# Kernel optimization log

Hardware: AMD Instinct MI355X
Metric: run time of the kernel (lower is better)

The kernel has to match this reference:

```python
import jax, jax.numpy as jnp
import numpy as np

B, H, N, D, R, HIDDEN = 4, 12, 1025, 64, 1, 32


def _make_tables(N, R):
    # Geometry tables, mirroring FlexAttentionCPB.init_tables
    P = N - R
    S = int(P ** 0.5)
    assert S * S == P
    rng = np.arange(-(S - 1), S, dtype=np.float32)        # [2S-1]
    dY, dX = np.meshgrid(rng, rng, indexing='ij')
    rel = np.stack([dY / max(S - 1, 1), dX / max(S - 1, 1)], axis=-1).reshape(-1, 2)
    rel_table = np.sign(rel) * np.log1p(np.abs(rel))      # [(2S-1)^2, 2]
    yy = np.arange(S)
    Y, X = np.meshgrid(yy, yy, indexing='ij')
    flat = np.stack([Y, X], 0).reshape(2, -1)             # [2, P]
    d = (flat[:, :, None] - flat[:, None, :]).transpose(1, 2, 0).copy()  # [P,P,2]
    d[:, :, 0] += S - 1
    d[:, :, 1] += S - 1
    d[:, :, 0] *= 2 * S - 1
    l_idx = d.sum(-1).astype(np.int32)
    idx = np.full((N, N), -1, dtype=np.int32)
    idx[R:, R:] = l_idx
    return jnp.asarray(rel_table, jnp.float32), jnp.asarray(idx)


def setup_inputs() -> dict:
    key = jax.random.key(0)
    ks = jax.random.split(key, 8)
    rel_table, idx_table = _make_tables(N, R)
    return {
        'q': jax.random.normal(ks[0], (B, H, N, D), jnp.float32),
        'k': jax.random.normal(ks[1], (B, H, N, D), jnp.float32),
        'v': jax.random.normal(ks[2], (B, H, N, D), jnp.float32),
        'mu': jax.random.normal(ks[3], (B, H, 2, N), jnp.float32),
        'w1': jax.random.normal(ks[4], (2, HIDDEN), jnp.float32) * 0.5,
        'b1': jax.random.normal(ks[5], (HIDDEN,), jnp.float32) * 0.05,
        'w2': jax.random.normal(ks[6], (HIDDEN, H), jnp.float32) * 0.1,
        'gamma': jnp.zeros((H,), jnp.float32),   # nn.Parameter(torch.zeros(H))
        'rel_table': rel_table,
        'idx_table': idx_table,
    }


def reference(q, k, v, mu, w1, b1, w2, gamma, rel_table, idx_table):
    d = q.shape[-1]
    # CPB MLP: Linear(2,hidden)+GELU(exact)+Linear(hidden,H,no bias) -> [L,H]
    bt = jax.nn.gelu(rel_table @ w1 + b1, approximate=False) @ w2
    has_bias = (idx_table >= 0)                       # [N,N] == (q>=R)&(kv>=R)
    idx_c = jnp.where(has_bias, idx_table, 0)
    bias = jnp.transpose(bt[idx_c], (2, 0, 1))        # [H,N,N]
    mu_q = mu[:, :, 0, :]                             # [B,H,N]
    mu_k = mu[:, :, 1, :]
    gate = jax.nn.sigmoid(gamma)[None, :, None, None] * (
        mu_q[..., :, None] + mu_k[..., None, :])      # [B,H,N,N]
    scale = 1.0 / jnp.sqrt(jnp.asarray(d, q.dtype))
    scores = jnp.einsum('bhqd,bhkd->bhqk', q, k) * scale
    scores = scores + has_bias[None, None].astype(scores.dtype) * gate * bias[None]
    attn = jax.nn.softmax(scores, axis=-1)
    return jnp.einsum('bhqk,bhkd->bhqd', attn, v)
```

## Files before the change

### kernel.cpp

```cpp
#include <hip/hip_runtime.h>
#include <math.h>

#define B_ 4
#define H_ 12
#define N_ 1025
#define D_ 64
#define HID_ 32
#define TBL_ 3969
#define NQT 17
#define NBLK (B_ * H_ * NQT)
#define LOG2E 1.44269504f
#define THR_ 12.0f

typedef _Float16 half8 __attribute__((ext_vector_type(8)));
typedef __fp16 fp16x2 __attribute__((ext_vector_type(2)));
typedef float f32x4 __attribute__((ext_vector_type(4)));

#if defined(__has_builtin)
#if __has_builtin(__builtin_amdgcn_exp2f)
#define EX2 __builtin_amdgcn_exp2f
#else
#define EX2 exp2f
#endif
#else
#define EX2 exp2f
#endif

#define BTT_OFF 0
#define AKT_OFF 190512
#define KF_OFF 399408
#define VF_OFF 7084080

__device__ __forceinline__ void stage16(const _Float16* gsrc, _Float16* ldst) {
    __builtin_amdgcn_global_load_lds(
        (const __attribute__((address_space(1))) void*)gsrc,
        (__attribute__((address_space(3))) void*)ldst, 16, 0, 0);
}

__global__ __launch_bounds__(256) void prep(
    const float* __restrict__ K, const float* __restrict__ V,
    const float* __restrict__ MU, const float* __restrict__ GAMMA,
    const float* __restrict__ rel, const float* __restrict__ w1,
    const float* __restrict__ b1, const float* __restrict__ w2,
    _Float16* __restrict__ Kf, _Float16* __restrict__ Vf,
    float* __restrict__ akT, float* __restrict__ btT) {
    const int bid = blockIdx.x;
    const int tid = threadIdx.x;
    if (bid < NBLK) {
        __shared__ float Vls[64 * 65];
        const int bh = bid / NQT, kt = bid % NQT;
        const size_t base = (size_t)bh * (N_ * D_);
        const int k0 = kt * 64;
#pragma unroll
        for (int it = 0; it < 4; ++it) {
            const int idx = it * 256 + tid;
            const int kr = idx >> 4, c4 = (idx & 15) << 2;
            const int kg = k0 + kr;
            float4 v4 = make_float4(0, 0, 0, 0);
            if (kg < N_) v4 = *(const float4*)(V + base + (size_t)kg * D_ + c4);
            Vls[(c4 + 0) * 65 + kr] = v4.x;
            Vls[(c4 + 1) * 65 + kr] = v4.y;
            Vls[(c4 + 2) * 65 + kr] = v4.z;
            Vls[(c4 + 3) * 65 + kr] = v4.w;
        }
        __syncthreads();
        const int lane = tid & 63, lq = lane & 15, g = lane >> 4;
        const int fbh = tid >> 6;
        const size_t tb = (size_t)(bh * NQT + kt) * 4096;
#pragma unroll
        for (int x = 0; x < 2; ++x) {
            const int fb = fbh + x * 4;
            {
                const int kh = fb >> 2, dg = fb & 3;
                const float* vp = &Vls[(dg * 16 + lq) * 65 + kh * 32 + g * 8];
                half8 v8;
#pragma unroll
                for (int j = 0; j < 8; ++j) v8[j] = (_Float16)vp[j];
                *(half8*)&Vf[tb + fb * 512 + lane * 8] = v8;
            }
            {
                const int row = k0 + (fb >> 1) * 16 + lq;
                const int col = (fb & 1) * 32 + g * 8;
                half8 k8;
                if (row < N_) {
                    const float4* p = (const float4*)(K + base + (size_t)row * D_ + col);
                    float4 a = p[0], b = p[1];
                    k8[0] = (_Float16)a.x; k8[1] = (_Float16)a.y;
                    k8[2] = (_Float16)a.z; k8[3] = (_Float16)a.w;
                    k8[4] = (_Float16)b.x; k8[5] = (_Float16)b.y;
                    k8[6] = (_Float16)b.z; k8[7] = (_Float16)b.w;
                } else {
#pragma unroll
                    for (int j = 0; j < 8; ++j) k8[j] = (_Float16)0.f;
                }
                *(half8*)&Kf[tb + fb * 512 + lane * 8] = k8;
            }
        }
        if (tid < 64) {
            const int kk = k0 + tid;
            const int h = bh % H_;
            const float sgl = LOG2E / (1.f + __expf(-GAMMA[h]));
            float a = 0.f;
            if (kk >= 1 && kk < N_) a = sgl * MU[((size_t)bh * 2 + 1) * N_ + kk];
            akT[bh * 1088 + kk] = a;
        }
    } else {
        const int i = (bid - NBLK) * 256 + tid;
        if (i < TBL_) {
            const float x0 = rel[2 * i + 0], x1 = rel[2 * i + 1];
            float acc[H_];
#pragma unroll
            for (int h = 0; h < H_; ++h) acc[h] = 0.f;
#pragma unroll
            for (int j = 0; j < HID_; ++j) {
                float t = fmaf(x0, w1[j], fmaf(x1, w1[HID_ + j], b1[j]));
                float gl = 0.5f * t * (1.f + erff(t * 0.7071067811865475f));
#pragma unroll
                for (int h = 0; h < H_; ++h) acc[h] = fmaf(gl, w2[j * H_ + h], acc[h]);
            }
#pragma unroll
            for (int h = 0; h < H_; ++h) btT[h * TBL_ + i] = acc[h];
        }
    }
}

__global__ __launch_bounds__(256, 4) void flex_attn(
    const float* __restrict__ Q, const _Float16* __restrict__ Kf,
    const _Float16* __restrict__ Vf, const float* __restrict__ MU,
    const float* __restrict__ GAMMA, const char* __restrict__ btb,
    const float* __restrict__ akT, float* __restrict__ OUT) {
    __shared__ __align__(16) _Float16 Ks[2][4096];
    __shared__ __align__(16) _Float16 Vs[2][4096];
    __shared__ __align__(16) _Float16 Pl[4][1024];

    const int bid = blockIdx.x;
    const int swz0 = (bid & 7) * (NBLK / 8) + (bid >> 3);
    const int bh = swz0 / NQT;
    const int qt = swz0 % NQT;
    const int h = bh % H_;
    const int tid = threadIdx.x;
    const int w = tid >> 6;
    const int lane = tid & 63;
    const int lq = lane & 15;
    const int g = lane >> 4;

    const size_t base = (size_t)bh * (N_ * D_);
    const float sg = LOG2E / (1.f + __expf(-GAMMA[h]));

    const int qrow = qt * 64 + w * 16 + lq;
    const bool qv = qrow < N_;

    half8 qf[2];
#pragma unroll
    for (int dh = 0; dh < 2; ++dh) {
        float4 t0 = make_float4(0, 0, 0, 0), t1 = t0;
        if (qv) {
            const float4* qp = (const float4*)(Q + base + (size_t)qrow * D_ + dh * 32 + g * 8);
            t0 = qp[0]; t1 = qp[1];
        }
        const float qs = 0.125f * LOG2E;
        half8 q8;
        q8[0] = (_Float16)(t0.x * qs); q8[1] = (_Float16)(t0.y * qs);
        q8[2] = (_Float16)(t0.z * qs); q8[3] = (_Float16)(t0.w * qs);
        q8[4] = (_Float16)(t1.x * qs); q8[5] = (_Float16)(t1.y * qs);
        q8[6] = (_Float16)(t1.z * qs); q8[7] = (_Float16)(t1.w * qs);
        qf[dh] = q8;
    }

    const bool qb = qv && (qrow >= 1);
    const float qbf = qb ? 1.f : 0.f;
    float aq = 0.f;
    int cq = 0;
    if (qb) {
        const int pq = qrow - 1;
        cq = (pq >> 5) * 63 + (pq & 31);
        aq = sg * MU[(size_t)bh * 2 * N_ + qrow];
    }
    int boffs[16];
#pragma unroll
    for (int kg = 0; kg < 4; ++kg) {
#pragma unroll
        for (int r = 0; r < 4; ++r) {
            const int pk = kg * 16 + g * 4 + r - 1;
            const int ck = (pk >> 5) * 63 + (pk & 31);
            boffs[kg * 4 + r] = (h * TBL_ + cq + 1984 - ck) * 4 + 2048;
        }
    }
    const float* akb = akT + bh * 1088;
    const _Float16* kfb = Kf + (size_t)bh * NQT * 4096;
    const _Float16* vfb = Vf + (size_t)bh * NQT * 4096;

    f32x4 o[4];
    const f32x4 zz = {0.f, 0.f, 0.f, 0.f};
#pragma unroll
    for (int dg = 0; dg < 4; ++dg) o[dg] = zz;
    float m = 0.f, lsum = 0.f;

    stage16(kfb + (2 * w + 0) * 512 + lane * 8, &Ks[0][(2 * w + 0) * 512]);
    stage16(kfb + (2 * w + 1) * 512 + lane * 8, &Ks[0][(2 * w + 1) * 512]);
    stage16(vfb + (2 * w + 0) * 512 + lane * 8, &Vs[0][(2 * w + 0) * 512]);
    stage16(vfb + (2 * w + 1) * 512 + lane * 8, &Vs[0][(2 * w + 1) * 512]);
    __syncthreads();

    const int pswz = (lq & 7) << 4;
    char* plw = (char*)&Pl[w][0];

    for (int t = 0; t < NQT; ++t) {
        const int buf = t & 1;
        const int kt0 = t * 64;

        float bt16[16];
#pragma unroll
        for (int i = 0; i < 16; ++i) {
            int off = boffs[i];
            off = off < 2048 ? 2048 : off;
            bt16[i] = *(const float*)(btb + (uint32_t)off);
            boffs[i] -= 504;
        }
        f32x4 akq[4];
#pragma unroll
        for (int kg = 0; kg < 4; ++kg)
            akq[kg] = *(const f32x4*)(akb + kt0 + kg * 16 + g * 4);

        if (t + 1 < NQT) {
            const _Float16* kn = kfb + (size_t)(t + 1) * 4096;
            const _Float16* vn = vfb + (size_t)(t + 1) * 4096;
            stage16(kn + (2 * w + 0) * 512 + lane * 8, &Ks[buf ^ 1][(2 * w + 0) * 512]);
            stage16(kn + (2 * w + 1) * 512 + lane * 8, &Ks[buf ^ 1][(2 * w + 1) * 512]);
            stage16(vn + (2 * w + 0) * 512 + lane * 8, &Vs[buf ^ 1][(2 * w + 0) * 512]);
            stage16(vn + (2 * w + 1) * 512 + lane * 8, &Vs[buf ^ 1][(2 * w + 1) * 512]);
        }

        const _Float16* ksl = &Ks[buf][lane * 8];
        f32x4 sa[4];
#pragma unroll
        for (int kg = 0; kg < 4; ++kg) {
            half8 a0 = *(const half8*)(ksl + (2 * kg + 0) * 512);
            half8 a1 = *(const half8*)(ksl + (2 * kg + 1) * 512);
            f32x4 z = zz;
            z = __builtin_amdgcn_mfma_f32_16x16x32_f16(a0, qf[0], z, 0, 0, 0);
            z = __builtin_amdgcn_mfma_f32_16x16x32_f16(a1, qf[1], z, 0, 0, 0);
            sa[kg] = z;
        }

        if (t == 0 && g == 0) bt16[0] = 0.f;
        float s[16];
#pragma unroll
        for (int kg = 0; kg < 4; ++kg) {
#pragma unroll
            for (int r = 0; r < 4; ++r) {
                const int i = kg * 4 + r;
                s[i] = fmaf(fmaf(qbf, akq[kg][r], aq), bt16[i], sa[kg][r]);
            }
        }
        if (t == NQT - 1) {
#pragma unroll
            for (int kg = 0; kg < 4; ++kg)
#pragma unroll
                for (int r = 0; r < 4; ++r) {
                    const int i = kg * 4 + r;
                    if (1024 + kg * 16 + g * 4 + r >= N_) s[i] = -1e30f;
                }
        }

        float lmax = s[0];
#pragma unroll
        for (int i = 1; i < 16; ++i) lmax = fmaxf(lmax, s[i]);
        if (t == 0) {
            float mt = fmaxf(lmax, __shfl_xor(lmax, 16));
            m = fmaxf(mt, __shfl_xor(mt, 32));
        } else if (!__all(lmax <= m + THR_)) {
            float mt = fmaxf(lmax, __shfl_xor(lmax, 16));
            mt = fmaxf(mt, __shfl_xor(mt, 32));
            const float mnew = fmaxf(m, mt);
            const float cc = EX2(m - mnew);
            m = mnew;
            lsum *= cc;
            float cc4[4];
#pragma unroll
            for (int r = 0; r < 4; ++r) cc4[r] = __shfl(cc, g * 4 + r);
#pragma unroll
            for (int dg = 0; dg < 4; ++dg)
#pragma unroll
                for (int r = 0; r < 4; ++r) o[dg][r] *= cc4[r];
        }
        float pv16[16];
        float ls0 = 0.f, ls1 = 0.f;
#pragma unroll
        for (int i = 0; i < 16; i += 2) {
            pv16[i] = EX2(s[i] - m);
            pv16[i + 1] = EX2(s[i + 1] - m);
            ls0 += pv16[i];
            ls1 += pv16[i + 1];
        }
        lsum += ls0 + ls1;

#pragma unroll
        for (int kg = 0; kg < 4; ++kg) {
            fp16x2 h0 = __builtin_amdgcn_cvt_pkrtz(pv16[kg * 4 + 0], pv16[kg * 4 + 1]);
            fp16x2 h1 = __builtin_amdgcn_cvt_pkrtz(pv16[kg * 4 + 2], pv16[kg * 4 + 3]);
            uint2 u = make_uint2(__builtin_bit_cast(uint32_t, h0),
                                 __builtin_bit_cast(uint32_t, h1));
            *(uint2*)(plw + lq * 128 + ((kg * 32 + g * 8) ^ pswz)) = u;
        }

#pragma unroll
        for (int kh = 0; kh < 2; ++kh) {
            half8 pa = *(const half8*)(plw + lq * 128 + ((kh * 64 + g * 16) ^ pswz));
#pragma unroll
            for (int dg = 0; dg < 4; ++dg) {
                half8 vb8 = *(const half8*)&Vs[buf][(kh * 4 + dg) * 512 + lane * 8];
                o[dg] = __builtin_amdgcn_mfma_f32_16x16x32_f16(pa, vb8, o[dg], 0, 0, 0);
            }
        }
        __syncthreads();
    }

    lsum += __shfl_xor(lsum, 16);
    lsum += __shfl_xor(lsum, 32);
    const float linv = 1.f / lsum;
    float li4[4];
#pragma unroll
    for (int r = 0; r < 4; ++r) li4[r] = __shfl(linv, g * 4 + r);
#pragma unroll
    for (int dg = 0; dg < 4; ++dg) {
#pragma unroll
        for (int r = 0; r < 4; ++r) {
            const int qq = qt * 64 + w * 16 + g * 4 + r;
            if (qq < N_) OUT[base + (size_t)qq * D_ + dg * 16 + lq] = o[dg][r] * li4[r];
        }
    }
}

extern "C" void kernel_launch(void* const* d_in, const int* in_sizes, int n_in,
                              void* d_out, int out_size, void* d_ws, size_t ws_size,
                              hipStream_t stream) {
    const float* q = (const float*)d_in[0];
    const float* k = (const float*)d_in[1];
    const float* v = (const float*)d_in[2];
    const float* mu = (const float*)d_in[3];
    const float* w1 = (const float*)d_in[4];
    const float* b1 = (const float*)d_in[5];
    const float* w2 = (const float*)d_in[6];
    const float* gamma = (const float*)d_in[7];
    const float* rel = (const float*)d_in[8];

    char* ws = (char*)d_ws;
    float* btT = (float*)(ws + BTT_OFF);
    float* akT = (float*)(ws + AKT_OFF);
    _Float16* Kf = (_Float16*)(ws + KF_OFF);
    _Float16* Vf = (_Float16*)(ws + VF_OFF);

    prep<<<NBLK + (TBL_ + 255) / 256, 256, 0, stream>>>(k, v, mu, gamma, rel, w1, b1, w2,
                                                        Kf, Vf, akT, btT);
    flex_attn<<<NBLK, 256, 0, stream>>>(q, Kf, Vf, mu, gamma, ws - 2048, akT, (float*)d_out);
}
```

Before: 65.81 us.

## Load K/V fragments directly into registers instead of staging through LDS

Drops the double-buffered LDS staging of K and V tiles and the per-tile block barrier. Each wave now loads its MFMA fragments straight from global memory into registers, with K prefetched one tile ahead via ping-pong register arrays in a loop unrolled by two. Launch bounds go from 4 to 2 blocks per CU to make room for the extra registers. This removes LDS traffic and synchronisation, but every wave now fetches the full K/V tile from global or L2 memory on its own, and occupancy may fall.

```diff
diff --git a/kernel.cpp b/kernel.cpp
--- a/kernel.cpp
+++ b/kernel.cpp
@@ -30,12 +30,6 @@
 #define AKT_OFF 190512
 #define KF_OFF 399408
 #define VF_OFF 7084080
-
-__device__ __forceinline__ void stage16(const _Float16* gsrc, _Float16* ldst) {
-    __builtin_amdgcn_global_load_lds(
-        (const __attribute__((address_space(1))) void*)gsrc,
-        (__attribute__((address_space(3))) void*)ldst, 16, 0, 0);
-}
 
 __global__ __launch_bounds__(256) void prep(
     const float* __restrict__ K, const float* __restrict__ V,
@@ -124,13 +118,11 @@
     }
 }
 
-__global__ __launch_bounds__(256, 4) void flex_attn(
+__global__ __launch_bounds__(256, 2) void flex_attn(
     const float* __restrict__ Q, const _Float16* __restrict__ Kf,
     const _Float16* __restrict__ Vf, const float* __restrict__ MU,
     const float* __restrict__ GAMMA, const char* __restrict__ btb,
     const float* __restrict__ akT, float* __restrict__ OUT) {
-    __shared__ __align__(16) _Float16 Ks[2][4096];
-    __shared__ __align__(16) _Float16 Vs[2][4096];
     __shared__ __align__(16) _Float16 Pl[4][1024];
 
     const int bid = blockIdx.x;
@@ -187,8 +179,8 @@
         }
     }
     const float* akb = akT + bh * 1088;
-    const _Float16* kfb = Kf + (size_t)bh * NQT * 4096;
-    const _Float16* vfb = Vf + (size_t)bh * NQT * 4096;
+    const _Float16* kfb = Kf + (size_t)bh * NQT * 4096 + lane * 8;
+    const _Float16* vfb = Vf + (size_t)bh * NQT * 4096 + lane * 8;
 
     f32x4 o[4];
     const f32x4 zz = {0.f, 0.f, 0.f, 0.f};
@@ -196,125 +188,114 @@
     for (int dg = 0; dg < 4; ++dg) o[dg] = zz;
     float m = 0.f, lsum = 0.f;
 
-    stage16(kfb + (2 * w + 0) * 512 + lane * 8, &Ks[0][(2 * w + 0) * 512]);
-    stage16(kfb + (2 * w + 1) * 512 + lane * 8, &Ks[0][(2 * w + 1) * 512]);
-    stage16(vfb + (2 * w + 0) * 512 + lane * 8, &Vs[0][(2 * w + 0) * 512]);
-    stage16(vfb + (2 * w + 1) * 512 + lane * 8, &Vs[0][(2 * w + 1) * 512]);
-    __syncthreads();
-
     const int pswz = (lq & 7) << 4;
     char* plw = (char*)&Pl[w][0];
 
-    for (int t = 0; t < NQT; ++t) {
-        const int buf = t & 1;
-        const int kt0 = t * 64;
-
-        float bt16[16];
-#pragma unroll
-        for (int i = 0; i < 16; ++i) {
-            int off = boffs[i];
-            off = off < 2048 ? 2048 : off;
-            bt16[i] = *(const float*)(btb + (uint32_t)off);
-            boffs[i] -= 504;
-        }
-        f32x4 akq[4];
-#pragma unroll
-        for (int kg = 0; kg < 4; ++kg)
-            akq[kg] = *(const f32x4*)(akb + kt0 + kg * 16 + g * 4);
-
-        if (t + 1 < NQT) {
-            const _Float16* kn = kfb + (size_t)(t + 1) * 4096;
-            const _Float16* vn = vfb + (size_t)(t + 1) * 4096;
-            stage16(kn + (2 * w + 0) * 512 + lane * 8, &Ks[buf ^ 1][(2 * w + 0) * 512]);
-            stage16(kn + (2 * w + 1) * 512 + lane * 8, &Ks[buf ^ 1][(2 * w + 1) * 512]);
-            stage16(vn + (2 * w + 0) * 512 + lane * 8, &Vs[buf ^ 1][(2 * w + 0) * 512]);
-            stage16(vn + (2 * w + 1) * 512 + lane * 8, &Vs[buf ^ 1][(2 * w + 1) * 512]);
-        }
-
-        const _Float16* ksl = &Ks[buf][lane * 8];
-        f32x4 sa[4];
-#pragma unroll
-        for (int kg = 0; kg < 4; ++kg) {
-            half8 a0 = *(const half8*)(ksl + (2 * kg + 0) * 512);
-            half8 a1 = *(const half8*)(ksl + (2 * kg + 1) * 512);
-            f32x4 z = zz;
-            z = __builtin_amdgcn_mfma_f32_16x16x32_f16(a0, qf[0], z, 0, 0, 0);
-            z = __builtin_amdgcn_mfma_f32_16x16x32_f16(a1, qf[1], z, 0, 0, 0);
-            sa[kg] = z;
-        }
-
-        if (t == 0 && g == 0) bt16[0] = 0.f;
-        float s[16];
-#pragma unroll
-        for (int kg = 0; kg < 4; ++kg) {
-#pragma unroll
-            for (int r = 0; r < 4; ++r) {
-                const int i = kg * 4 + r;
-                s[i] = fmaf(fmaf(qbf, akq[kg][r], aq), bt16[i], sa[kg][r]);
-            }
-        }
-        if (t == NQT - 1) {
-#pragma unroll
-            for (int kg = 0; kg < 4; ++kg)
-#pragma unroll
-                for (int r = 0; r < 4; ++r) {
-                    const int i = kg * 4 + r;
-                    if (1024 + kg * 16 + g * 4 + r >= N_) s[i] = -1e30f;
-                }
-        }
-
-        float lmax = s[0];
-#pragma unroll
-        for (int i = 1; i < 16; ++i) lmax = fmaxf(lmax, s[i]);
-        if (t == 0) {
-            float mt = fmaxf(lmax, __shfl_xor(lmax, 16));
-            m = fmaxf(mt, __shfl_xor(mt, 32));
-        } else if (!__all(lmax <= m + THR_)) {
-            float mt = fmaxf(lmax, __shfl_xor(lmax, 16));
-            mt = fmaxf(mt, __shfl_xor(mt, 32));
-            const float mnew = fmaxf(m, mt);
-            const float cc = EX2(m - mnew);
-            m = mnew;
-            lsum *= cc;
-            float cc4[4];
-#pragma unroll
-            for (int r = 0; r < 4; ++r) cc4[r] = __shfl(cc, g * 4 + r);
-#pragma unroll
-            for (int dg = 0; dg < 4; ++dg)
-#pragma unroll
-                for (int r = 0; r < 4; ++r) o[dg][r] *= cc4[r];
-        }
-        float pv16[16];
-        float ls0 = 0.f, ls1 = 0.f;
-#pragma unroll
-        for (int i = 0; i < 16; i += 2) {
-            pv16[i] = EX2(s[i] - m);
-            pv16[i + 1] = EX2(s[i + 1] - m);
-            ls0 += pv16[i];
-            ls1 += pv16[i + 1];
-        }
-        lsum += ls0 + ls1;
-
-#pragma unroll
-        for (int kg = 0; kg < 4; ++kg) {
-            fp16x2 h0 = __builtin_amdgcn_cvt_pkrtz(pv16[kg * 4 + 0], pv16[kg * 4 + 1]);
-            fp16x2 h1 = __builtin_amdgcn_cvt_pkrtz(pv16[kg * 4 + 2], pv16[kg * 4 + 3]);
-            uint2 u = make_uint2(__builtin_bit_cast(uint32_t, h0),
-                                 __builtin_bit_cast(uint32_t, h1));
-            *(uint2*)(plw + lq * 128 + ((kg * 32 + g * 8) ^ pswz)) = u;
-        }
-
-#pragma unroll
-        for (int kh = 0; kh < 2; ++kh) {
-            half8 pa = *(const half8*)(plw + lq * 128 + ((kh * 64 + g * 16) ^ pswz));
-#pragma unroll
-            for (int dg = 0; dg < 4; ++dg) {
-                half8 vb8 = *(const half8*)&Vs[buf][(kh * 4 + dg) * 512 + lane * 8];
-                o[dg] = __builtin_amdgcn_mfma_f32_16x16x32_f16(pa, vb8, o[dg], 0, 0, 0);
-            }
-        }
-        __syncthreads();
-    }
+    half8 kA[8], kB[8], vv[8];
+#pragma unroll
+    for (int f = 0; f < 8; ++f) kA[f] = *(const half8*)(kfb + f * 512);
+
+#define TILE_BODY(KC, KN, TT, DO_PRE)                                                   \
+    {                                                                                   \
+        const int t_ = (TT);                                                            \
+                \
+        {                                                                               \
+            const _Float16* vp_ = vfb + (size_t)t_ * 4096;                              \
+            _Pragma("unroll") for (int f = 0; f < 8; ++f)                               \
+                vv[f] = *(const half8*)(vp_ + f * 512);                                 \
+        }                                                                               \
+         \
+        float bt16[16];                                                                 \
+        _Pragma("unroll") for (int i = 0; i < 16; ++i) {                                \
+            int off = boffs[i];                                                         \
+            off = off < 2048 ? 2048 : off;                                              \
+            bt16[i] = *(const float*)(btb + (uint32_t)off);                             \
+            boffs[i] -= 504;                                                            \
+        }                                                                               \
+        f32x4 akq[4];                                                                   \
+        _Pragma("unroll") for (int kg = 0; kg < 4; ++kg)                                \
+            akq[kg] = *(const f32x4*)(akb + t_ * 64 + kg * 16 + g * 4);                 \
+                                                           \
+        f32x4 sa[4];                                                                    \
+        _Pragma("unroll") for (int kg = 0; kg < 4; ++kg) {                              \
+            f32x4 z = zz;                                                               \
+            z = __builtin_amdgcn_mfma_f32_16x16x32_f16(KC[2 * kg + 0], qf[0], z, 0, 0, 0); \
+            z = __builtin_amdgcn_mfma_f32_16x16x32_f16(KC[2 * kg + 1], qf[1], z, 0, 0, 0); \
+            sa[kg] = z;                                                                 \
+        }                                                                               \
+                                                  \
+        if (DO_PRE) {                                                                   \
+            const _Float16* kp_ = kfb + (size_t)(t_ + 1) * 4096;                        \
+            _Pragma("unroll") for (int f = 0; f < 8; ++f)                               \
+                KN[f] = *(const half8*)(kp_ + f * 512);                                 \
+        }                                                                               \
+                                   \
+        if (t_ == 0 && g == 0) bt16[0] = 0.f;               \
+        float s[16];                                                                    \
+        _Pragma("unroll") for (int kg = 0; kg < 4; ++kg) {                              \
+            _Pragma("unroll") for (int r = 0; r < 4; ++r) {                             \
+                const int i = kg * 4 + r;                                               \
+                s[i] = fmaf(fmaf(qbf, akq[kg][r], aq), bt16[i], sa[kg][r]);             \
+            }                                                                           \
+        }                                                                               \
+        if (t_ == NQT - 1) {                                           \
+            _Pragma("unroll") for (int kg = 0; kg < 4; ++kg)                            \
+                _Pragma("unroll") for (int r = 0; r < 4; ++r) {                         \
+                    if (1024 + kg * 16 + g * 4 + r >= N_) s[kg * 4 + r] = -1e30f;       \
+                }                                                                       \
+        }                                                                               \
+                   \
+        float lmax = s[0];                                                              \
+        _Pragma("unroll") for (int i = 1; i < 16; ++i) lmax = fmaxf(lmax, s[i]);        \
+        if (t_ == 0) {                                                                  \
+            float mt = fmaxf(lmax, __shfl_xor(lmax, 16));                               \
+            m = fmaxf(mt, __shfl_xor(mt, 32));                                          \
+        } else if (!__all(lmax <= m + THR_)) {                                          \
+            float mt = fmaxf(lmax, __shfl_xor(lmax, 16));                               \
+            mt = fmaxf(mt, __shfl_xor(mt, 32));                                         \
+            const float mnew = fmaxf(m, mt);                                            \
+            const float cc = EX2(m - mnew);                                             \
+            m = mnew;                                                                   \
+            lsum *= cc;                                                                 \
+            float cc4[4];                                                               \
+            _Pragma("unroll") for (int r = 0; r < 4; ++r) cc4[r] = __shfl(cc, g * 4 + r); \
+            _Pragma("unroll") for (int dg = 0; dg < 4; ++dg)                            \
+                _Pragma("unroll") for (int r = 0; r < 4; ++r) o[dg][r] *= cc4[r];       \
+        }                                                                               \
+        float pv16[16];                                                                 \
+        float ls0 = 0.f, ls1 = 0.f;                                                     \
+        _Pragma("unroll") for (int i = 0; i < 16; i += 2) {                             \
+            pv16[i] = EX2(s[i] - m);                                                    \
+            pv16[i + 1] = EX2(s[i + 1] - m);                                            \
+            ls0 += pv16[i];                                                             \
+            ls1 += pv16[i + 1];                                                         \
+        }                                                                               \
+        lsum += ls0 + ls1;                                                              \
+                  \
+        _Pragma("unroll") for (int kg = 0; kg < 4; ++kg) {                              \
+            fp16x2 h0 = __builtin_amdgcn_cvt_pkrtz(pv16[kg * 4 + 0], pv16[kg * 4 + 1]); \
+            fp16x2 h1 = __builtin_amdgcn_cvt_pkrtz(pv16[kg * 4 + 2], pv16[kg * 4 + 3]); \
+            uint2 u = make_uint2(__builtin_bit_cast(uint32_t, h0),                      \
+                                 __builtin_bit_cast(uint32_t, h1));                     \
+            *(uint2*)(plw + lq * 128 + ((kg * 32 + g * 8) ^ pswz)) = u;                 \
+        }                                                                               \
+                                                    \
+        _Pragma("unroll") for (int kh = 0; kh < 2; ++kh) {                              \
+            half8 pa = *(const half8*)(plw + lq * 128 + ((kh * 64 + g * 16) ^ pswz));   \
+            _Pragma("unroll") for (int dg = 0; dg < 4; ++dg) {                          \
+                o[dg] = __builtin_amdgcn_mfma_f32_16x16x32_f16(pa, vv[kh * 4 + dg],     \
+                                                               o[dg], 0, 0, 0);        \
+            }                                                                           \
+        }                                                                               \
+    }
+
+#pragma unroll 1
+    for (int tt = 0; tt < NQT - 1; tt += 2) {
+        TILE_BODY(kA, kB, tt, 1)
+        TILE_BODY(kB, kA, tt + 1, 1)
+    }
+    TILE_BODY(kA, kB, NQT - 1, 0)
+#undef TILE_BODY
 
     lsum += __shfl_xor(lsum, 16);
     lsum += __shfl_xor(lsum, 32);
```

New measurement: 81.41 us. 23.7% more time.

## Triple-buffer K/V staging in attention and hoist K loads in prep

Applied to the files above, without the earlier changes.

The attention kernel moves from double- to triple-buffered LDS staging of the K/V tiles, prefetching two tiles ahead. It replaces __syncthreads with a raw s_barrier plus an explicit vmcnt wait and sched barriers, and relaxes launch bounds from 4 to 2 blocks per CU to fit the larger LDS footprint. The prep kernel issues its K global loads before the V transpose so both sets of loads are in flight together. The goal is to hide global-load latency behind MFMA work, at the cost of fewer resident blocks per CU. The hand-managed waitcnt and barriers also risk ordering bugs, since bias loads share the vmcnt counter with the tile loads.

```diff
diff --git a/kernel.cpp b/kernel.cpp
--- a/kernel.cpp
+++ b/kernel.cpp
@@ -51,6 +51,23 @@
         const int bh = bid / NQT, kt = bid % NQT;
         const size_t base = (size_t)bh * (N_ * D_);
         const int k0 = kt * 64;
+        const int lane = tid & 63, lq = lane & 15, g = lane >> 4;
+        const int fbh = tid >> 6;
+        const size_t tb = (size_t)(bh * NQT + kt) * 4096;
+        float4 kld[2][2];
+#pragma unroll
+        for (int x = 0; x < 2; ++x) {
+            const int fb = fbh + x * 4;
+            const int row = k0 + (fb >> 1) * 16 + lq;
+            const int col = (fb & 1) * 32 + g * 8;
+            kld[x][0] = make_float4(0, 0, 0, 0);
+            kld[x][1] = kld[x][0];
+            if (row < N_) {
+                const float4* p = (const float4*)(K + base + (size_t)row * D_ + col);
+                kld[x][0] = p[0];
+                kld[x][1] = p[1];
+            }
+        }
 #pragma unroll
         for (int it = 0; it < 4; ++it) {
             const int idx = it * 256 + tid;
@@ -64,9 +81,6 @@
             Vls[(c4 + 3) * 65 + kr] = v4.w;
         }
         __syncthreads();
-        const int lane = tid & 63, lq = lane & 15, g = lane >> 4;
-        const int fbh = tid >> 6;
-        const size_t tb = (size_t)(bh * NQT + kt) * 4096;
 #pragma unroll
         for (int x = 0; x < 2; ++x) {
             const int fb = fbh + x * 4;
@@ -79,20 +93,12 @@
                 *(half8*)&Vf[tb + fb * 512 + lane * 8] = v8;
             }
             {
-                const int row = k0 + (fb >> 1) * 16 + lq;
-                const int col = (fb & 1) * 32 + g * 8;
                 half8 k8;
-                if (row < N_) {
-                    const float4* p = (const float4*)(K + base + (size_t)row * D_ + col);
-                    float4 a = p[0], b = p[1];
-                    k8[0] = (_Float16)a.x; k8[1] = (_Float16)a.y;
-                    k8[2] = (_Float16)a.z; k8[3] = (_Float16)a.w;
-                    k8[4] = (_Float16)b.x; k8[5] = (_Float16)b.y;
-                    k8[6] = (_Float16)b.z; k8[7] = (_Float16)b.w;
-                } else {
-#pragma unroll
-                    for (int j = 0; j < 8; ++j) k8[j] = (_Float16)0.f;
-                }
+                float4 a = kld[x][0], b = kld[x][1];
+                k8[0] = (_Float16)a.x; k8[1] = (_Float16)a.y;
+                k8[2] = (_Float16)a.z; k8[3] = (_Float16)a.w;
+                k8[4] = (_Float16)b.x; k8[5] = (_Float16)b.y;
+                k8[6] = (_Float16)b.z; k8[7] = (_Float16)b.w;
                 *(half8*)&Kf[tb + fb * 512 + lane * 8] = k8;
             }
         }
@@ -124,13 +130,13 @@
     }
 }
 
-__global__ __launch_bounds__(256, 4) void flex_attn(
+__global__ __launch_bounds__(256, 2) void flex_attn(
     const float* __restrict__ Q, const _Float16* __restrict__ Kf,
     const _Float16* __restrict__ Vf, const float* __restrict__ MU,
     const float* __restrict__ GAMMA, const char* __restrict__ btb,
     const float* __restrict__ akT, float* __restrict__ OUT) {
-    __shared__ __align__(16) _Float16 Ks[2][4096];
-    __shared__ __align__(16) _Float16 Vs[2][4096];
+    __shared__ __align__(16) _Float16 Ks[3][4096];
+    __shared__ __align__(16) _Float16 Vs[3][4096];
     __shared__ __align__(16) _Float16 Pl[4][1024];
 
     const int bid = blockIdx.x;
@@ -196,17 +202,25 @@
     for (int dg = 0; dg < 4; ++dg) o[dg] = zz;
     float m = 0.f, lsum = 0.f;
 
-    stage16(kfb + (2 * w + 0) * 512 + lane * 8, &Ks[0][(2 * w + 0) * 512]);
-    stage16(kfb + (2 * w + 1) * 512 + lane * 8, &Ks[0][(2 * w + 1) * 512]);
-    stage16(vfb + (2 * w + 0) * 512 + lane * 8, &Vs[0][(2 * w + 0) * 512]);
-    stage16(vfb + (2 * w + 1) * 512 + lane * 8, &Vs[0][(2 * w + 1) * 512]);
-    __syncthreads();
-
     const int pswz = (lq & 7) << 4;
     char* plw = (char*)&Pl[w][0];
 
+#pragma unroll
+    for (int t0 = 0; t0 < 2; ++t0) {
+        const _Float16* kp = kfb + (size_t)t0 * 4096;
+        const _Float16* vp = vfb + (size_t)t0 * 4096;
+        stage16(kp + (2 * w + 0) * 512 + lane * 8, &Ks[t0][(2 * w + 0) * 512]);
+        stage16(kp + (2 * w + 1) * 512 + lane * 8, &Ks[t0][(2 * w + 1) * 512]);
+        stage16(vp + (2 * w + 0) * 512 + lane * 8, &Vs[t0][(2 * w + 0) * 512]);
+        stage16(vp + (2 * w + 1) * 512 + lane * 8, &Vs[t0][(2 * w + 1) * 512]);
+    }
+    asm volatile("s_waitcnt vmcnt(4)" ::: "memory");
+    __builtin_amdgcn_sched_barrier(0);
+    __builtin_amdgcn_s_barrier();
+
+    int cur = 0, stg = 2;
+#pragma unroll 1
     for (int t = 0; t < NQT; ++t) {
-        const int buf = t & 1;
         const int kt0 = t * 64;
 
         float bt16[16];
@@ -221,17 +235,18 @@
 #pragma unroll
         for (int kg = 0; kg < 4; ++kg)
             akq[kg] = *(const f32x4*)(akb + kt0 + kg * 16 + g * 4);
-
-        if (t + 1 < NQT) {
-            const _Float16* kn = kfb + (size_t)(t + 1) * 4096;
-            const _Float16* vn = vfb + (size_t)(t + 1) * 4096;
-            stage16(kn + (2 * w + 0) * 512 + lane * 8, &Ks[buf ^ 1][(2 * w + 0) * 512]);
-            stage16(kn + (2 * w + 1) * 512 + lane * 8, &Ks[buf ^ 1][(2 * w + 1) * 512]);
-            stage16(vn + (2 * w + 0) * 512 + lane * 8, &Vs[buf ^ 1][(2 * w + 0) * 512]);
-            stage16(vn + (2 * w + 1) * 512 + lane * 8, &Vs[buf ^ 1][(2 * w + 1) * 512]);
-        }
-
-        const _Float16* ksl = &Ks[buf][lane * 8];
+        __builtin_amdgcn_sched_barrier(0);
+
+        if (t + 2 < NQT) {
+            const _Float16* kn = kfb + (size_t)(t + 2) * 4096;
+            const _Float16* vn = vfb + (size_t)(t + 2) * 4096;
+            stage16(kn + (2 * w + 0) * 512 + lane * 8, &Ks[stg][(2 * w + 0) * 512]);
+            stage16(kn + (2 * w + 1) * 512 + lane * 8, &Ks[stg][(2 * w + 1) * 512]);
+            stage16(vn + (2 * w + 0) * 512 + lane * 8, &Vs[stg][(2 * w + 0) * 512]);
+            stage16(vn + (2 * w + 1) * 512 + lane * 8, &Vs[stg][(2 * w + 1) * 512]);
+        }
+
+        const _Float16* ksl = &Ks[cur][lane * 8];
         f32x4 sa[4];
 #pragma unroll
         for (int kg = 0; kg < 4; ++kg) {
@@ -309,11 +324,13 @@
             half8 pa = *(const half8*)(plw + lq * 128 + ((kh * 64 + g * 16) ^ pswz));
 #pragma unroll
             for (int dg = 0; dg < 4; ++dg) {
-                half8 vb8 = *(const half8*)&Vs[buf][(kh * 4 + dg) * 512 + lane * 8];
+                half8 vb8 = *(const half8*)&Vs[cur][(kh * 4 + dg) * 512 + lane * 8];
                 o[dg] = __builtin_amdgcn_mfma_f32_16x16x32_f16(pa, vb8, o[dg], 0, 0, 0);
             }
         }
-        __syncthreads();
+        __builtin_amdgcn_s_barrier();
+        cur = (cur == 2) ? 0 : cur + 1;
+        stg = (stg == 2) ? 0 : stg + 1;
     }
 
     lsum += __shfl_xor(lsum, 16);
```

Result: slower. 76.28 us (+15.9%).

## Process two 16-row query subtiles per wave and halve attention block size

Applied to the files above, without the earlier changes.

The attention kernel now runs 128 threads per block, and each wave handles 32 query rows as two 16-row subtiles. Each K and V fragment loaded from LDS feeds twice as many MFMAs, and each block still covers 64 query rows. The prep kernel packs V to fp16 pairs before the LDS transpose and hoists the K loads ahead of the V staging. In exchange, register pressure roughly doubles (two accumulator sets and two softmax states), and fewer waves are resident to hide latency.

```diff
diff --git a/kernel.cpp b/kernel.cpp
--- a/kernel.cpp
+++ b/kernel.cpp
@@ -37,6 +37,11 @@
         (__attribute__((address_space(3))) void*)ldst, 16, 0, 0);
 }
 
+__device__ __forceinline__ uint32_t pk2(float a, float b) {
+    fp16x2 t = __builtin_amdgcn_cvt_pkrtz(a, b);
+    return __builtin_bit_cast(uint32_t, t);
+}
+
 __global__ __launch_bounds__(256) void prep(
     const float* __restrict__ K, const float* __restrict__ V,
     const float* __restrict__ MU, const float* __restrict__ GAMMA,
@@ -47,52 +52,57 @@
     const int bid = blockIdx.x;
     const int tid = threadIdx.x;
     if (bid < NBLK) {
-        __shared__ float Vls[64 * 65];
+        __shared__ uint32_t VlsU[64 * 36];
         const int bh = bid / NQT, kt = bid % NQT;
         const size_t base = (size_t)bh * (N_ * D_);
         const int k0 = kt * 64;
-#pragma unroll
-        for (int it = 0; it < 4; ++it) {
-            const int idx = it * 256 + tid;
-            const int kr = idx >> 4, c4 = (idx & 15) << 2;
-            const int kg = k0 + kr;
-            float4 v4 = make_float4(0, 0, 0, 0);
-            if (kg < N_) v4 = *(const float4*)(V + base + (size_t)kg * D_ + c4);
-            Vls[(c4 + 0) * 65 + kr] = v4.x;
-            Vls[(c4 + 1) * 65 + kr] = v4.y;
-            Vls[(c4 + 2) * 65 + kr] = v4.z;
-            Vls[(c4 + 3) * 65 + kr] = v4.w;
-        }
-        __syncthreads();
         const int lane = tid & 63, lq = lane & 15, g = lane >> 4;
         const int fbh = tid >> 6;
         const size_t tb = (size_t)(bh * NQT + kt) * 4096;
+        float4 kld[2][2];
+#pragma unroll
+        for (int x = 0; x < 2; ++x) {
+            const int fb = fbh + x * 4;
+            const int row = k0 + (fb >> 1) * 16 + lq;
+            const int col = (fb & 1) * 32 + g * 8;
+            kld[x][0] = make_float4(0, 0, 0, 0);
+            kld[x][1] = kld[x][0];
+            if (row < N_) {
+                const float4* p = (const float4*)(K + base + (size_t)row * D_ + col);
+                kld[x][0] = p[0];
+                kld[x][1] = p[1];
+            }
+        }
+#pragma unroll
+        for (int it = 0; it < 2; ++it) {
+            const int idx = it * 256 + tid;
+            const int p = idx >> 4;
+            const int c4 = (idx & 15) << 2;
+            const int r0 = k0 + 2 * p;
+            float4 a = make_float4(0, 0, 0, 0), b = a;
+            if (r0 < N_) a = *(const float4*)(V + base + (size_t)r0 * D_ + c4);
+            if (r0 + 1 < N_) b = *(const float4*)(V + base + (size_t)(r0 + 1) * D_ + c4);
+            VlsU[(c4 + 0) * 36 + p] = pk2(a.x, b.x);
+            VlsU[(c4 + 1) * 36 + p] = pk2(a.y, b.y);
+            VlsU[(c4 + 2) * 36 + p] = pk2(a.z, b.z);
+            VlsU[(c4 + 3) * 36 + p] = pk2(a.w, b.w);
+        }
+        __syncthreads();
 #pragma unroll
         for (int x = 0; x < 2; ++x) {
             const int fb = fbh + x * 4;
             {
                 const int kh = fb >> 2, dg = fb & 3;
-                const float* vp = &Vls[(dg * 16 + lq) * 65 + kh * 32 + g * 8];
-                half8 v8;
-#pragma unroll
-                for (int j = 0; j < 8; ++j) v8[j] = (_Float16)vp[j];
-                *(half8*)&Vf[tb + fb * 512 + lane * 8] = v8;
+                uint4 u = *(const uint4*)&VlsU[(dg * 16 + lq) * 36 + kh * 16 + g * 4];
+                *(uint4*)&Vf[tb + fb * 512 + lane * 8] = u;
             }
             {
-                const int row = k0 + (fb >> 1) * 16 + lq;
-                const int col = (fb & 1) * 32 + g * 8;
                 half8 k8;
-                if (row < N_) {
-                    const float4* p = (const float4*)(K + base + (size_t)row * D_ + col);
-                    float4 a = p[0], b = p[1];
-                    k8[0] = (_Float16)a.x; k8[1] = (_Float16)a.y;
-                    k8[2] = (_Float16)a.z; k8[3] = (_Float16)a.w;
-                    k8[4] = (_Float16)b.x; k8[5] = (_Float16)b.y;
-                    k8[6] = (_Float16)b.z; k8[7] = (_Float16)b.w;
-                } else {
-#pragma unroll
-                    for (int j = 0; j < 8; ++j) k8[j] = (_Float16)0.f;
-                }
+                float4 a = kld[x][0], b = kld[x][1];
+                k8[0] = (_Float16)a.x; k8[1] = (_Float16)a.y;
+                k8[2] = (_Float16)a.z; k8[3] = (_Float16)a.w;
+                k8[4] = (_Float16)b.x; k8[5] = (_Float16)b.y;
+                k8[6] = (_Float16)b.z; k8[7] = (_Float16)b.w;
                 *(half8*)&Kf[tb + fb * 512 + lane * 8] = k8;
             }
         }
@@ -124,14 +134,14 @@
     }
 }
 
-__global__ __launch_bounds__(256, 4) void flex_attn(
+__global__ __launch_bounds__(128, 2) void flex_attn(
     const float* __restrict__ Q, const _Float16* __restrict__ Kf,
     const _Float16* __restrict__ Vf, const float* __restrict__ MU,
     const float* __restrict__ GAMMA, const char* __restrict__ btb,
     const float* __restrict__ akT, float* __restrict__ OUT) {
     __shared__ __align__(16) _Float16 Ks[2][4096];
     __shared__ __align__(16) _Float16 Vs[2][4096];
-    __shared__ __align__(16) _Float16 Pl[4][1024];
+    __shared__ __align__(16) _Float16 Pl[2][2][1024];
 
     const int bid = blockIdx.x;
     const int swz0 = (bid & 7) * (NBLK / 8) + (bid >> 3);
@@ -147,34 +157,48 @@
     const size_t base = (size_t)bh * (N_ * D_);
     const float sg = LOG2E / (1.f + __expf(-GAMMA[h]));
 
-    const int qrow = qt * 64 + w * 16 + lq;
-    const bool qv = qrow < N_;
-
-    half8 qf[2];
-#pragma unroll
-    for (int dh = 0; dh < 2; ++dh) {
-        float4 t0 = make_float4(0, 0, 0, 0), t1 = t0;
-        if (qv) {
-            const float4* qp = (const float4*)(Q + base + (size_t)qrow * D_ + dh * 32 + g * 8);
-            t0 = qp[0]; t1 = qp[1];
-        }
-        const float qs = 0.125f * LOG2E;
-        half8 q8;
-        q8[0] = (_Float16)(t0.x * qs); q8[1] = (_Float16)(t0.y * qs);
-        q8[2] = (_Float16)(t0.z * qs); q8[3] = (_Float16)(t0.w * qs);
-        q8[4] = (_Float16)(t1.x * qs); q8[5] = (_Float16)(t1.y * qs);
-        q8[6] = (_Float16)(t1.z * qs); q8[7] = (_Float16)(t1.w * qs);
-        qf[dh] = q8;
-    }
-
-    const bool qb = qv && (qrow >= 1);
-    const float qbf = qb ? 1.f : 0.f;
-    float aq = 0.f;
-    int cq = 0;
-    if (qb) {
-        const int pq = qrow - 1;
-        cq = (pq >> 5) * 63 + (pq & 31);
-        aq = sg * MU[(size_t)bh * 2 * N_ + qrow];
+    const int qrow0 = qt * 64 + w * 32 + lq;
+    const int qrow1 = qrow0 + 16;
+    const bool qv0 = qrow0 < N_;
+    const bool qv1 = qrow1 < N_;
+
+    half8 qf0[2], qf1[2];
+#pragma unroll
+    for (int sub = 0; sub < 2; ++sub) {
+        const int qr = sub ? qrow1 : qrow0;
+        const bool v = sub ? qv1 : qv0;
+#pragma unroll
+        for (int dh = 0; dh < 2; ++dh) {
+            float4 t0 = make_float4(0, 0, 0, 0), t1 = t0;
+            if (v) {
+                const float4* qp = (const float4*)(Q + base + (size_t)qr * D_ + dh * 32 + g * 8);
+                t0 = qp[0]; t1 = qp[1];
+            }
+            const float qs = 0.125f * LOG2E;
+            half8 q8;
+            q8[0] = (_Float16)(t0.x * qs); q8[1] = (_Float16)(t0.y * qs);
+            q8[2] = (_Float16)(t0.z * qs); q8[3] = (_Float16)(t0.w * qs);
+            q8[4] = (_Float16)(t1.x * qs); q8[5] = (_Float16)(t1.y * qs);
+            q8[6] = (_Float16)(t1.z * qs); q8[7] = (_Float16)(t1.w * qs);
+            if (sub) qf1[dh] = q8; else qf0[dh] = q8;
+        }
+    }
+
+    const bool qb0 = qv0 && (qrow0 >= 1);
+    const bool qb1 = qv1;
+    const float qbf0 = qb0 ? 1.f : 0.f;
+    const float qbf1 = qb1 ? 1.f : 0.f;
+    float aq0 = 0.f, aq1 = 0.f;
+    int cq0 = 0, cq1 = 0;
+    if (qb0) {
+        const int pq = qrow0 - 1;
+        cq0 = (pq >> 5) * 63 + (pq & 31);
+        aq0 = sg * MU[(size_t)bh * 2 * N_ + qrow0];
+    }
+    if (qb1) {
+        const int pq = qrow1 - 1;
+        cq1 = (pq >> 5) * 63 + (pq & 31);
+        aq1 = sg * MU[(size_t)bh * 2 * N_ + qrow1];
     }
     int boffs[16];
 #pragma unroll
@@ -183,38 +207,45 @@
         for (int r = 0; r < 4; ++r) {
             const int pk = kg * 16 + g * 4 + r - 1;
             const int ck = (pk >> 5) * 63 + (pk & 31);
-            boffs[kg * 4 + r] = (h * TBL_ + cq + 1984 - ck) * 4 + 2048;
-        }
-    }
+            boffs[kg * 4 + r] = (h * TBL_ + cq0 + 1984 - ck) * 4 + 2048;
+        }
+    }
+    const int dB = (cq1 - cq0) * 4;
     const float* akb = akT + bh * 1088;
     const _Float16* kfb = Kf + (size_t)bh * NQT * 4096;
     const _Float16* vfb = Vf + (size_t)bh * NQT * 4096;
 
-    f32x4 o[4];
+    f32x4 o0[4], o1[4];
     const f32x4 zz = {0.f, 0.f, 0.f, 0.f};
 #pragma unroll
-    for (int dg = 0; dg < 4; ++dg) o[dg] = zz;
-    float m = 0.f, lsum = 0.f;
-
-    stage16(kfb + (2 * w + 0) * 512 + lane * 8, &Ks[0][(2 * w + 0) * 512]);
-    stage16(kfb + (2 * w + 1) * 512 + lane * 8, &Ks[0][(2 * w + 1) * 512]);
-    stage16(vfb + (2 * w + 0) * 512 + lane * 8, &Vs[0][(2 * w + 0) * 512]);
-    stage16(vfb + (2 * w + 1) * 512 + lane * 8, &Vs[0][(2 * w + 1) * 512]);
+    for (int dg = 0; dg < 4; ++dg) { o0[dg] = zz; o1[dg] = zz; }
+    float m0 = 0.f, l0 = 0.f, m1 = 0.f, l1 = 0.f;
+
+    const int pswz = (lq & 7) << 4;
+    char* plw0 = (char*)&Pl[w][0][0];
+    char* plw1 = (char*)&Pl[w][1][0];
+
+#pragma unroll
+    for (int c = 0; c < 4; ++c) {
+        stage16(kfb + (4 * w + c) * 512 + lane * 8, &Ks[0][(4 * w + c) * 512]);
+        stage16(vfb + (4 * w + c) * 512 + lane * 8, &Vs[0][(4 * w + c) * 512]);
+    }
     __syncthreads();
 
-    const int pswz = (lq & 7) << 4;
-    char* plw = (char*)&Pl[w][0];
-
+#pragma unroll 1
     for (int t = 0; t < NQT; ++t) {
         const int buf = t & 1;
         const int kt0 = t * 64;
 
-        float bt16[16];
+        float btA[16], btB[16];
 #pragma unroll
         for (int i = 0; i < 16; ++i) {
-            int off = boffs[i];
-            off = off < 2048 ? 2048 : off;
-            bt16[i] = *(const float*)(btb + (uint32_t)off);
+            int offA = boffs[i];
+            int offB = offA + dB;
+            offA = offA < 2048 ? 2048 : offA;
+            offB = offB < 2048 ? 2048 : offB;
+            btA[i] = *(const float*)(btb + (uint32_t)offA);
+            btB[i] = *(const float*)(btb + (uint32_t)offB);
             boffs[i] -= 504;
         }
         f32x4 akq[4];
@@ -225,109 +256,114 @@
         if (t + 1 < NQT) {
             const _Float16* kn = kfb + (size_t)(t + 1) * 4096;
             const _Float16* vn = vfb + (size_t)(t + 1) * 4096;
-            stage16(kn + (2 * w + 0) * 512 + lane * 8, &Ks[buf ^ 1][(2 * w + 0) * 512]);
-            stage16(kn + (2 * w + 1) * 512 + lane * 8, &Ks[buf ^ 1][(2 * w + 1) * 512]);
-            stage16(vn + (2 * w + 0) * 512 + lane * 8, &Vs[buf ^ 1][(2 * w + 0) * 512]);
-            stage16(vn + (2 * w + 1) * 512 + lane * 8, &Vs[buf ^ 1][(2 * w + 1) * 512]);
+#pragma unroll
+            for (int c = 0; c < 4; ++c) {
+                stage16(kn + (4 * w + c) * 512 + lane * 8, &Ks[buf ^ 1][(4 * w + c) * 512]);
+                stage16(vn + (4 * w + c) * 512 + lane * 8, &Vs[buf ^ 1][(4 * w + c) * 512]);
+            }
         }
 
         const _Float16* ksl = &Ks[buf][lane * 8];
-        f32x4 sa[4];
+        f32x4 sa0[4], sa1[4];
 #pragma unroll
         for (int kg = 0; kg < 4; ++kg) {
             half8 a0 = *(const half8*)(ksl + (2 * kg + 0) * 512);
             half8 a1 = *(const half8*)(ksl + (2 * kg + 1) * 512);
-            f32x4 z = zz;
-            z = __builtin_amdgcn_mfma_f32_16x16x32_f16(a0, qf[0], z, 0, 0, 0);
-            z = __builtin_amdgcn_mfma_f32_16x16x32_f16(a1, qf[1], z, 0, 0, 0);
-            sa[kg] = z;
-        }
-
-        if (t == 0 && g == 0) bt16[0] = 0.f;
-        float s[16];
-#pragma unroll
-        for (int kg = 0; kg < 4; ++kg) {
-#pragma unroll
-            for (int r = 0; r < 4; ++r) {
-                const int i = kg * 4 + r;
-                s[i] = fmaf(fmaf(qbf, akq[kg][r], aq), bt16[i], sa[kg][r]);
-            }
-        }
-        if (t == NQT - 1) {
-#pragma unroll
-            for (int kg = 0; kg < 4; ++kg)
-#pragma unroll
-                for (int r = 0; r < 4; ++r) {
-                    const int i = kg * 4 + r;
-                    if (1024 + kg * 16 + g * 4 + r >= N_) s[i] = -1e30f;
-                }
-        }
-
-        float lmax = s[0];
-#pragma unroll
-        for (int i = 1; i < 16; ++i) lmax = fmaxf(lmax, s[i]);
-        if (t == 0) {
-            float mt = fmaxf(lmax, __shfl_xor(lmax, 16));
-            m = fmaxf(mt, __shfl_xor(mt, 32));
-        } else if (!__all(lmax <= m + THR_)) {
-            float mt = fmaxf(lmax, __shfl_xor(lmax, 16));
-            mt = fmaxf(mt, __shfl_xor(mt, 32));
-            const float mnew = fmaxf(m, mt);
-            const float cc = EX2(m - mnew);
-            m = mnew;
-            lsum *= cc;
-            float cc4[4];
-#pragma unroll
-            for (int r = 0; r < 4; ++r) cc4[r] = __shfl(cc, g * 4 + r);
-#pragma unroll
-            for (int dg = 0; dg < 4; ++dg)
-#pragma unroll
-                for (int r = 0; r < 4; ++r) o[dg][r] *= cc4[r];
-        }
-        float pv16[16];
-        float ls0 = 0.f, ls1 = 0.f;
-#pragma unroll
-        for (int i = 0; i < 16; i += 2) {
-            pv16[i] = EX2(s[i] - m);
-            pv16[i + 1] = EX2(s[i + 1] - m);
-            ls0 += pv16[i];
-            ls1 += pv16[i + 1];
-        }
-        lsum += ls0 + ls1;
-
-#pragma unroll
-        for (int kg = 0; kg < 4; ++kg) {
-            fp16x2 h0 = __builtin_amdgcn_cvt_pkrtz(pv16[kg * 4 + 0], pv16[kg * 4 + 1]);
-            fp16x2 h1 = __builtin_amdgcn_cvt_pkrtz(pv16[kg * 4 + 2], pv16[kg * 4 + 3]);
-            uint2 u = make_uint2(__builtin_bit_cast(uint32_t, h0),
-                                 __builtin_bit_cast(uint32_t, h1));
-            *(uint2*)(plw + lq * 128 + ((kg * 32 + g * 8) ^ pswz)) = u;
-        }
+            f32x4 z0 = zz, z1 = zz;
+            z0 = __builtin_amdgcn_mfma_f32_16x16x32_f16(a0, qf0[0], z0, 0, 0, 0);
+            z1 = __builtin_amdgcn_mfma_f32_16x16x32_f16(a0, qf1[0], z1, 0, 0, 0);
+            z0 = __builtin_amdgcn_mfma_f32_16x16x32_f16(a1, qf0[1], z0, 0, 0, 0);
+            z1 = __builtin_amdgcn_mfma_f32_16x16x32_f16(a1, qf1[1], z1, 0, 0, 0);
+            sa0[kg] = z0;
+            sa1[kg] = z1;
+        }
+
+        if (t == 0 && g == 0) { btA[0] = 0.f; btB[0] = 0.f; }
+
+#define SOFTMAX_SUB(SA, BT, QBF, AQ, MM, LL, OO, PLW)                                  \
+    {                                                                                  \
+        float s[16];                                                                   \
+        _Pragma("unroll") for (int kg = 0; kg < 4; ++kg) {                             \
+            _Pragma("unroll") for (int r = 0; r < 4; ++r) {                            \
+                const int i = kg * 4 + r;                                              \
+                s[i] = fmaf(fmaf(QBF, akq[kg][r], AQ), BT[i], SA[kg][r]);              \
+            }                                                                          \
+        }                                                                              \
+        if (t == NQT - 1) {                                                            \
+            _Pragma("unroll") for (int kg = 0; kg < 4; ++kg)                           \
+                _Pragma("unroll") for (int r = 0; r < 4; ++r) {                        \
+                    if (1024 + kg * 16 + g * 4 + r >= N_) s[kg * 4 + r] = -1e30f;      \
+                }                                                                      \
+        }                                                                              \
+        float lmax = s[0];                                                             \
+        _Pragma("unroll") for (int i = 1; i < 16; ++i) lmax = fmaxf(lmax, s[i]);       \
+        if (t == 0) {                                                                  \
+            float mt = fmaxf(lmax, __shfl_xor(lmax, 16));                              \
+            MM = fmaxf(mt, __shfl_xor(mt, 32));                                        \
+        } else if (!__all(lmax <= MM + THR_)) {                                        \
+            float mt = fmaxf(lmax, __shfl_xor(lmax, 16));                              \
+            mt = fmaxf(mt, __shfl_xor(mt, 32));                                        \
+            const float mnew = fmaxf(MM, mt);                                          \
+            const float cc = EX2(MM - mnew);                                           \
+            MM = mnew;                                                                 \
+            LL *= cc;                                                                  \
+            float cc4[4];                                                              \
+            _Pragma("unroll") for (int r = 0; r < 4; ++r) cc4[r] = __shfl(cc, g * 4 + r); \
+            _Pragma("unroll") for (int dg = 0; dg < 4; ++dg)                           \
+                _Pragma("unroll") for (int r = 0; r < 4; ++r) OO[dg][r] *= cc4[r];     \
+        }                                                                              \
+        float pv16[16];                                                                \
+        float ls0 = 0.f, ls1 = 0.f;                                                    \
+        _Pragma("unroll") for (int i = 0; i < 16; i += 2) {                            \
+            pv16[i] = EX2(s[i] - MM);                                                  \
+            pv16[i + 1] = EX2(s[i + 1] - MM);                                          \
+            ls0 += pv16[i];                                                            \
+            ls1 += pv16[i + 1];                                                        \
+        }                                                                              \
+        LL += ls0 + ls1;                                                               \
+        _Pragma("unroll") for (int kg = 0; kg < 4; ++kg) {                             \
+            uint2 u = make_uint2(pk2(pv16[kg * 4 + 0], pv16[kg * 4 + 1]),              \
+                                 pk2(pv16[kg * 4 + 2], pv16[kg * 4 + 3]));             \
+            *(uint2*)(PLW + lq * 128 + ((kg * 32 + g * 8) ^ pswz)) = u;                \
+        }                                                                              \
+    }
+
+        SOFTMAX_SUB(sa0, btA, qbf0, aq0, m0, l0, o0, plw0)
+        SOFTMAX_SUB(sa1, btB, qbf1, aq1, m1, l1, o1, plw1)
+#undef SOFTMAX_SUB
 
 #pragma unroll
         for (int kh = 0; kh < 2; ++kh) {
-            half8 pa = *(const half8*)(plw + lq * 128 + ((kh * 64 + g * 16) ^ pswz));
+            half8 pa0 = *(const half8*)(plw0 + lq * 128 + ((kh * 64 + g * 16) ^ pswz));
+            half8 pa1 = *(const half8*)(plw1 + lq * 128 + ((kh * 64 + g * 16) ^ pswz));
 #pragma unroll
             for (int dg = 0; dg < 4; ++dg) {
                 half8 vb8 = *(const half8*)&Vs[buf][(kh * 4 + dg) * 512 + lane * 8];
-                o[dg] = __builtin_amdgcn_mfma_f32_16x16x32_f16(pa, vb8, o[dg], 0, 0, 0);
+                o0[dg] = __builtin_amdgcn_mfma_f32_16x16x32_f16(pa0, vb8, o0[dg], 0, 0, 0);
+                o1[dg] = __builtin_amdgcn_mfma_f32_16x16x32_f16(pa1, vb8, o1[dg], 0, 0, 0);
             }
         }
         __syncthreads();
     }
 
-    lsum += __shfl_xor(lsum, 16);
-    lsum += __shfl_xor(lsum, 32);
-    const float linv = 1.f / lsum;
-    float li4[4];
-#pragma unroll
-    for (int r = 0; r < 4; ++r) li4[r] = __shfl(linv, g * 4 + r);
+    l0 += __shfl_xor(l0, 16); l0 += __shfl_xor(l0, 32);
+    l1 += __shfl_xor(l1, 16); l1 += __shfl_xor(l1, 32);
+    const float li0 = 1.f / l0;
+    const float li1 = 1.f / l1;
+    float li4a[4], li4b[4];
+#pragma unroll
+    for (int r = 0; r < 4; ++r) {
+        li4a[r] = __shfl(li0, g * 4 + r);
+        li4b[r] = __shfl(li1, g * 4 + r);
+    }
 #pragma unroll
     for (int dg = 0; dg < 4; ++dg) {
 #pragma unroll
         for (int r = 0; r < 4; ++r) {
-            const int qq = qt * 64 + w * 16 + g * 4 + r;
-            if (qq < N_) OUT[base + (size_t)qq * D_ + dg * 16 + lq] = o[dg][r] * li4[r];
+            const int qq0 = qt * 64 + w * 32 + g * 4 + r;
+            if (qq0 < N_) OUT[base + (size_t)qq0 * D_ + dg * 16 + lq] = o0[dg][r] * li4a[r];
+            const int qq1 = qq0 + 16;
+            if (qq1 < N_) OUT[base + (size_t)qq1 * D_ + dg * 16 + lq] = o1[dg][r] * li4b[r];
         }
     }
 }
@@ -353,5 +389,5 @@
 
     prep<<<NBLK + (TBL_ + 255) / 256, 256, 0, stream>>>(k, v, mu, gamma, rel, w1, b1, w2,
                                                         Kf, Vf, akT, btT);
-    flex_attn<<<NBLK, 256, 0, stream>>>(q, Kf, Vf, mu, gamma, ws - 2048, akT, (float*)d_out);
-}
+    flex_attn<<<NBLK, 128, 0, stream>>>(q, Kf, Vf, mu, gamma, ws - 2048, akT, (float*)d_out);
+}
```

After: 73.88 us. 1.12x slower.
